# Kernel optimization log

Hardware: AMD Instinct MI355X
Metric: run time of the kernel (lower is better)

Reference implementation:

```python
import jax, jax.numpy as jnp
import numpy as np

K = 3        # kernel_size
STRIDE = 1
FILTER = 32
ATOM = 16    # output atom
B, H, W, C, IN_ATOM = 4, 16, 16, 32, 16


def kernel_tile(x, k, stride):
    # x: [B,H,W,C,A] -> [B,oh,ow,k*k*C,A]  (im2col patch gather, VALID padding)
    b, h, w, c, a = x.shape
    oh = (h - k) // stride + 1
    ow = (w - k) // stride + 1
    patches = jnp.stack(
        [x[:, i:i + stride * oh:stride, j:j + stride * ow:stride]
         for i in range(k) for j in range(k)],
        axis=3,
    )  # [B,oh,ow,k*k,C,A]
    return patches.reshape(b, oh, ow, k * k * c, a)


def setup_inputs() -> dict:
    key = jax.random.key(0)
    k1, k2 = jax.random.split(key)
    x = jax.random.normal(k1, (B, H, W, C, IN_ATOM), dtype=jnp.float32)
    # capsule_kernel: [k*k*in_channel, in_atom, filter*atom] (glorot-ish scale)
    matrix = jax.random.normal(k2, (K * K * C, IN_ATOM, FILTER * ATOM), dtype=jnp.float32) * 0.05
    return {"x": x, "matrix": matrix}


def reference(x, matrix):
    tile = kernel_tile(x, K, STRIDE)                      # [B,oh,ow,N,in_atom], N=k*k*C
    votes = jnp.einsum('bhwna,nac->bhwnc', tile, matrix)  # per-capsule matmul
    b, oh, ow, n, _ = votes.shape
    return votes.reshape(b, oh, ow, n, FILTER, ATOM)      # [B,oh,ow,k*k*C,filter,atom]
```

## Files before the change

### kernel.cpp

```cpp
#include <hip/hip_runtime.h>


#define KK      3
#define CIN     32
#define IN_ATOM 16
#define FC      512
#define OH      14
#define OW      14
#define BATCH   4
#define HH      16
#define WW      16
#define NN      (KK*KK*CIN)

__global__ __launch_bounds__(128, 2)
void caps_transform_kernel(const float* __restrict__ x,
                           const float* __restrict__ m,
                           float* __restrict__ out)
{
    const int n   = blockIdx.x;
    const int b   = blockIdx.y;
    const int fc0 = threadIdx.x * 4;

    const int ki = n / (KK * CIN);
    const int kj = (n / CIN) % KK;
    const int c  = n % CIN;

    float4 mm[IN_ATOM];
    const float* mp = m + ((long)n * IN_ATOM) * FC + fc0;
#pragma unroll
    for (int a = 0; a < IN_ATOM; ++a)
        mm[a] = *reinterpret_cast<const float4*>(mp + (long)a * FC);

    const float* xb = x + ((long)b * HH * WW * CIN + (long)c) * IN_ATOM;
    float* ob = out + ((long)b * OH * OW * NN + n) * (long)FC + fc0;

    for (int oh = 0; oh < OH; ++oh) {
        const float* xrow = xb + (long)(oh + ki) * WW * CIN * IN_ATOM;
        float* orow = ob + (long)oh * OW * (NN * FC);
        for (int ow = 0; ow < OW; ++ow) {
            const float* xp = xrow + (long)(ow + kj) * (CIN * IN_ATOM);
            float4 acc = make_float4(0.f, 0.f, 0.f, 0.f);
#pragma unroll
            for (int a = 0; a < IN_ATOM; ++a) {
                const float xv = xp[a];
                acc.x += xv * mm[a].x;
                acc.y += xv * mm[a].y;
                acc.z += xv * mm[a].z;
                acc.w += xv * mm[a].w;
            }
            *reinterpret_cast<float4*>(orow + (long)ow * (NN * FC)) = acc;
        }
    }
}

extern "C" void kernel_launch(void* const* d_in, const int* in_sizes, int n_in,
                              void* d_out, int out_size, void* d_ws, size_t ws_size,
                              hipStream_t stream)
{
    const float* x = (const float*)d_in[0];
    const float* m = (const float*)d_in[1];
    float* out = (float*)d_out;

    dim3 grid(NN, BATCH);
    dim3 block(128);
    caps_transform_kernel<<<grid, block, 0, stream>>>(x, m, out);
}
```

Before: 537.0 us.

## Split work per output row with wider blocks and XCD-aware block remapping

Grid changes from one block per (capsule, batch), each looping over all 14x14 positions, to one block per (capsule, batch, output row) with 256 threads producing two output floats each. Blocks are remapped so consecutive logical blocks land on the same XCD, and x values are preloaded per position before the FMA chain. This raises parallelism and occupancy for a store-bound kernel (about 94 MB of output), at the cost of reloading matrix values 14 times more often and using narrower float2 stores.

Result: slower. 986.1 us (+83.6%).

```diff
diff --git a/kernel.cpp b/kernel.cpp
--- a/kernel.cpp
+++ b/kernel.cpp
@@ -11,45 +11,50 @@
 #define HH      16
 #define WW      16
 #define NN      (KK*KK*CIN)
+#define NWG     (NN*BATCH*OH)
 
-__global__ __launch_bounds__(128, 2)
+__global__ __launch_bounds__(256, 8)
 void caps_transform_kernel(const float* __restrict__ x,
                            const float* __restrict__ m,
                            float* __restrict__ out)
 {
-    const int n   = blockIdx.x;
-    const int b   = blockIdx.y;
-    const int fc0 = threadIdx.x * 4;
+    const int orig    = blockIdx.x;
+    const int logical = (orig & 7) * (NWG / 8) + (orig >> 3);
 
-    const int ki = n / (KK * CIN);
-    const int kj = (n / CIN) % KK;
-    const int c  = n % CIN;
+    const int n   = logical / (BATCH * OH);
+    const int rem = logical % (BATCH * OH);
+    const int b   = rem / OH;
+    const int oh  = rem % OH;
 
-    float4 mm[IN_ATOM];
-    const float* mp = m + ((long)n * IN_ATOM) * FC + fc0;
+    const int fc0 = threadIdx.x * 2;
+    const int ki  = n / (KK * CIN);
+    const int kj  = (n / CIN) % KK;
+    const int c   = n % CIN;
+
+    float2 mm[IN_ATOM];
+    const float* mp = m + (n * IN_ATOM) * FC + fc0;
 #pragma unroll
     for (int a = 0; a < IN_ATOM; ++a)
-        mm[a] = *reinterpret_cast<const float4*>(mp + (long)a * FC);
+        mm[a] = *reinterpret_cast<const float2*>(mp + a * FC);
 
-    const float* xb = x + ((long)b * HH * WW * CIN + (long)c) * IN_ATOM;
-    float* ob = out + ((long)b * OH * OW * NN + n) * (long)FC + fc0;
+    const float* xrow = x + (((b * HH + (oh + ki)) * WW + kj) * CIN + c) * IN_ATOM;
+    float* orow = out + (((b * OH + oh) * OW) * NN + n) * FC + fc0;
 
-    for (int oh = 0; oh < OH; ++oh) {
-        const float* xrow = xb + (long)(oh + ki) * WW * CIN * IN_ATOM;
-        float* orow = ob + (long)oh * OW * (NN * FC);
-        for (int ow = 0; ow < OW; ++ow) {
-            const float* xp = xrow + (long)(ow + kj) * (CIN * IN_ATOM);
-            float4 acc = make_float4(0.f, 0.f, 0.f, 0.f);
+#pragma unroll 2
+    for (int ow = 0; ow < OW; ++ow) {
+        const float* xp = xrow + ow * (CIN * IN_ATOM);
+        float xv[IN_ATOM];
 #pragma unroll
-            for (int a = 0; a < IN_ATOM; ++a) {
-                const float xv = xp[a];
-                acc.x += xv * mm[a].x;
-                acc.y += xv * mm[a].y;
-                acc.z += xv * mm[a].z;
-                acc.w += xv * mm[a].w;
-            }
-            *reinterpret_cast<float4*>(orow + (long)ow * (NN * FC)) = acc;
+        for (int a = 0; a < IN_ATOM; ++a)
+            xv[a] = xp[a];
+
+        float2 acc = make_float2(0.f, 0.f);
+#pragma unroll
+        for (int a = 0; a < IN_ATOM; ++a) {
+            acc.x += xv[a] * mm[a].x;
+            acc.y += xv[a] * mm[a].y;
         }
+        *reinterpret_cast<float2*>(orow + ow * (NN * FC)) = acc;
     }
 }
 
@@ -61,7 +66,5 @@
     const float* m = (const float*)d_in[1];
     float* out = (float*)d_out;
 
-    dim3 grid(NN, BATCH);
-    dim3 block(128);
-    caps_transform_kernel<<<grid, block, 0, stream>>>(x, m, out);
+    caps_transform_kernel<<<dim3(NWG), dim3(256), 0, stream>>>(x, m, out);
 }
```
